# Kernel tuning notes

Measured on AMD Instinct MI355X. Metric: run time of the kernel, lower is better.

Reference implementation:

```python
import jax, jax.numpy as jnp
import numpy as np

N = 16384      # number of PF candidates (nodes)
D_IN = 13      # pfc_input_dim
H = 16         # hidden_dim
K = 8          # kNN neighbors (includes self, dist 0, matching PyG knn(x, x, k))


def setup_inputs() -> dict:
    key = jax.random.key(0)
    ks = jax.random.split(key, 8)

    def w(k, shape):
        return (jax.random.normal(k, shape, dtype=jnp.float32) * 0.1)

    z = lambda n: jnp.zeros((n,), dtype=jnp.float32)
    return {
        "x_pfc": jax.random.normal(ks[0], (N, D_IN), dtype=jnp.float32),
        # pfc_encode: Linear(13,8) SiLU, Linear(8,16) SiLU, Linear(16,15)
        "W1": w(ks[1], (D_IN, H // 2)), "b1": z(H // 2),
        "W2": w(ks[2], (H // 2, H)),    "b2": z(H),
        "W3": w(ks[3], (H, H - 1)),     "b3": z(H - 1),
        # DynamicEdgeConv edge MLP: Linear(2H, H) SiLU
        "We": w(ks[4], (2 * H, H)),     "be": z(H),
        # ffn: Linear(H, 2H) SiLU, Linear(2H, H)
        "Wf1": w(ks[5], (H, 2 * H)),    "bf1": z(2 * H),
        "Wf2": w(ks[6], (2 * H, H)),    "bf2": z(H),
    }


def reference(x_pfc, W1, b1, W2, b2, W3, b3, We, be, Wf1, bf1, Wf2, bf2):
    silu = jax.nn.silu
    # pfc_encode (dropout = identity in eval)
    h = silu(x_pfc @ W1 + b1)
    h = silu(h @ W2 + b2)
    h = h @ W3 + b3                                   # [N, H-1]
    x = jnp.concatenate([h, x_pfc[:, -1:]], axis=1)   # [N, H]

    # Dynamic kNN graph in encoded-feature space (self included, dist 0)
    sq = jnp.sum(x * x, axis=1)                       # [N]
    d2 = sq[:, None] + sq[None, :] - 2.0 * (x @ x.T)  # [N, N] pairwise sq dist
    _, idx = jax.lax.top_k(-d2, K)                    # [N, K] neighbor indices

    # EdgeConv message: nn(cat([x_i, x_j - x_i])), mean aggregation
    x_j = x[idx]                                      # [N, K, H] gather
    x_i = x[:, None, :]                               # [N, 1, H]
    edge_in = jnp.concatenate(
        [jnp.broadcast_to(x_i, x_j.shape), x_j - x_i], axis=-1)  # [N, K, 2H]
    msg = silu(edge_in @ We + be)                     # [N, K, H]
    feats = jnp.mean(msg, axis=1)                     # [N, H]

    # ffn (dropout = identity in eval)
    f = silu(feats @ Wf1 + bf1)
    f = f @ Wf2 + bf2                                 # [N, H]
    return jnp.concatenate([f, x_pfc], axis=1)        # [N, H + D_IN]
```

## Files before the change

kernel.cpp:

```cpp
#include <hip/hip_runtime.h>
#include <math.h>

#define NPTS 16384
#define DIN 13
#define KNN 8
#define GL 12
#define BIGF 1.7014118e38f

typedef _Float16 half8 __attribute__((ext_vector_type(8)));
typedef float f32x4 __attribute__((ext_vector_type(4)));
typedef float f32x16 __attribute__((ext_vector_type(16)));

union HU4 { uint4 u; half8 h; };

__device__ __forceinline__ float silu(float v) {
    return v / (1.0f + __expf(-v));
}

#define MED3(v, a, b) __builtin_amdgcn_fmed3f((v), (a), (b))

#define INS8V(v) {                      \
    d7 = MED3((v), d6, d7);             \
    d6 = MED3((v), d5, d6);             \
    d5 = MED3((v), d4, d5);             \
    d4 = MED3((v), d3, d4);             \
    d3 = MED3((v), d2, d3);             \
    d2 = MED3((v), d1, d2);             \
    d1 = MED3((v), d0, d1);             \
    d0 = fminf((v), d0); }

#define INS12G(v) {                     \
    g11 = MED3((v), g10, g11);          \
    g10 = MED3((v), g9, g10);           \
    g9  = MED3((v), g8, g9);            \
    g8  = MED3((v), g7, g8);            \
    g7  = MED3((v), g6, g7);            \
    g6  = MED3((v), g5, g6);            \
    g5  = MED3((v), g4, g5);            \
    g4  = MED3((v), g3, g4);            \
    g3  = MED3((v), g2, g3);            \
    g2  = MED3((v), g1, g2);            \
    g1  = MED3((v), g0, g1);            \
    g0  = fminf((v), g0); }

#define CSW(p, q) { float lo_ = fminf(m##p, m##q); float hi_ = fmaxf(m##p, m##q); m##p = lo_; m##q = hi_; }

#define CLEAN16() \
    CSW(0,8) CSW(1,9) CSW(2,10) CSW(3,11) CSW(4,12) CSW(5,13) CSW(6,14) CSW(7,15) \
    CSW(0,4) CSW(1,5) CSW(2,6) CSW(3,7) CSW(8,12) CSW(9,13) CSW(10,14) CSW(11,15) \
    CSW(0,2) CSW(1,3) CSW(4,6) CSW(5,7) CSW(8,10) CSW(9,11) CSW(12,14) CSW(13,15) \
    CSW(0,1) CSW(2,3) CSW(4,5) CSW(6,7) CSW(8,9) CSW(10,11) CSW(12,13) CSW(14,15)

#define MERGE12_SHFL(mask) {                                  \
    float b0 = __shfl_xor(g0, (mask), 64);                    \
    float b1 = __shfl_xor(g1, (mask), 64);                    \
    float b2 = __shfl_xor(g2, (mask), 64);                    \
    float b3 = __shfl_xor(g3, (mask), 64);                    \
    float b4 = __shfl_xor(g4, (mask), 64);                    \
    float b5 = __shfl_xor(g5, (mask), 64);                    \
    float b6 = __shfl_xor(g6, (mask), 64);                    \
    float b7 = __shfl_xor(g7, (mask), 64);                    \
    float b8 = __shfl_xor(g8, (mask), 64);                    \
    float b9 = __shfl_xor(g9, (mask), 64);                    \
    float b10 = __shfl_xor(g10, (mask), 64);                  \
    float b11 = __shfl_xor(g11, (mask), 64);                  \
    float m0 = g0, m1 = g1, m2 = g2, m3 = g3;                 \
    float m4 = fminf(g4, b11), m5 = fminf(g5, b10);           \
    float m6 = fminf(g6, b9),  m7 = fminf(g7, b8);            \
    float m8 = fminf(g8, b7),  m9 = fminf(g9, b6);            \
    float m10 = fminf(g10, b5), m11 = fminf(g11, b4);         \
    float m12 = b3, m13 = b2, m14 = b1, m15 = b0;             \
    CLEAN16();                                                \
    g0 = m0; g1 = m1; g2 = m2; g3 = m3; g4 = m4; g5 = m5;     \
    g6 = m6; g7 = m7; g8 = m8; g9 = m9; g10 = m10; g11 = m11; }

#define MERGE12_LDS(LD) {                                     \
    float b0 = LD(0), b1 = LD(1), b2 = LD(2), b3 = LD(3);     \
    float b4 = LD(4), b5 = LD(5), b6 = LD(6), b7 = LD(7);     \
    float b8 = LD(8), b9 = LD(9), b10 = LD(10), b11 = LD(11); \
    float m0 = g0, m1 = g1, m2 = g2, m3 = g3;                 \
    float m4 = fminf(g4, b11), m5 = fminf(g5, b10);           \
    float m6 = fminf(g6, b9),  m7 = fminf(g7, b8);            \
    float m8 = fminf(g8, b7),  m9 = fminf(g9, b6);            \
    float m10 = fminf(g10, b5), m11 = fminf(g11, b4);         \
    float m12 = b3, m13 = b2, m14 = b1, m15 = b0;             \
    CLEAN16();                                                \
    g0 = m0; g1 = m1; g2 = m2; g3 = m3; g4 = m4; g5 = m5;     \
    g6 = m6; g7 = m7; g8 = m8; g9 = m9; g10 = m10; g11 = m11; }

#define MERGE8(mask) {                                   \
    float b0 = __shfl_xor(d0, (mask), 64);               \
    float b1 = __shfl_xor(d1, (mask), 64);               \
    float b2 = __shfl_xor(d2, (mask), 64);               \
    float b3 = __shfl_xor(d3, (mask), 64);               \
    float b4 = __shfl_xor(d4, (mask), 64);               \
    float b5 = __shfl_xor(d5, (mask), 64);               \
    float b6 = __shfl_xor(d6, (mask), 64);               \
    float b7 = __shfl_xor(d7, (mask), 64);               \
    float m0 = fminf(d0, b7), m1 = fminf(d1, b6);        \
    float m2 = fminf(d2, b5), m3 = fminf(d3, b4);        \
    float m4 = fminf(d4, b3), m5 = fminf(d5, b2);        \
    float m6 = fminf(d6, b1), m7 = fminf(d7, b0);        \
    CSW(0,4) CSW(1,5) CSW(2,6) CSW(3,7)                  \
    CSW(0,2) CSW(1,3) CSW(4,6) CSW(5,7)                  \
    CSW(0,1) CSW(2,3) CSW(4,5) CSW(6,7)                  \
    d0 = m0; d1 = m1; d2 = m2; d3 = m3;                  \
    d4 = m4; d5 = m5; d6 = m6; d7 = m7; }

__global__ __launch_bounds__(64) void k_encoder(
    const float* __restrict__ x_pfc,
    const float* __restrict__ W1, const float* __restrict__ b1,
    const float* __restrict__ W2, const float* __restrict__ b2,
    const float* __restrict__ W3, const float* __restrict__ b3,
    const float* __restrict__ We, const float* __restrict__ be,
    float* __restrict__ xo, _Float16* __restrict__ H, _Float16* __restrict__ L,
    _Float16* __restrict__ YH, _Float16* __restrict__ YL,
    float* __restrict__ SQF, unsigned* __restrict__ SQHL,
    float* __restrict__ ACC)
{
    __shared__ float sW1[DIN * 8];
    __shared__ float sb1[8];
    __shared__ float sW2[8 * 16];
    __shared__ float sb2[16];
    __shared__ float sW3[16 * 15];
    __shared__ float sb3[15];
    __shared__ float sWe[16 * 16];
    __shared__ float sbe[16];
    int t = threadIdx.x;
    for (int q = t; q < DIN * 8; q += 64) sW1[q] = W1[q];
    for (int q = t; q < 8; q += 64) sb1[q] = b1[q];
    for (int q = t; q < 8 * 16; q += 64) sW2[q] = W2[q];
    for (int q = t; q < 16; q += 64) sb2[q] = b2[q];
    for (int q = t; q < 16 * 15; q += 64) sW3[q] = W3[q];
    for (int q = t; q < 15; q += 64) sb3[q] = b3[q];
    for (int q = t; q < 16 * 16; q += 64) sWe[q] = We[q];
    for (int q = t; q < 16; q += 64) sbe[q] = be[q];
    __syncthreads();

    int i = blockIdx.x * 64 + t;
    float in[DIN];
#pragma unroll
    for (int d = 0; d < DIN; ++d) in[d] = x_pfc[i * DIN + d];

    float a1[8];
#pragma unroll
    for (int h = 0; h < 8; ++h) a1[h] = sb1[h];
#pragma unroll
    for (int d = 0; d < DIN; ++d) {
        float v = in[d];
#pragma unroll
        for (int h = 0; h < 8; ++h) a1[h] += v * sW1[d * 8 + h];
    }
#pragma unroll
    for (int h = 0; h < 8; ++h) a1[h] = silu(a1[h]);

    float a2[16];
#pragma unroll
    for (int h = 0; h < 16; ++h) a2[h] = sb2[h];
#pragma unroll
    for (int d = 0; d < 8; ++d) {
        float v = a1[d];
#pragma unroll
        for (int h = 0; h < 16; ++h) a2[h] += v * sW2[d * 16 + h];
    }
#pragma unroll
    for (int h = 0; h < 16; ++h) a2[h] = silu(a2[h]);

    float a3[15];
#pragma unroll
    for (int h = 0; h < 15; ++h) a3[h] = sb3[h];
#pragma unroll
    for (int d = 0; d < 16; ++d) {
        float v = a2[d];
#pragma unroll
        for (int h = 0; h < 15; ++h) a3[h] += v * sW3[d * 15 + h];
    }

    float xr[16];
#pragma unroll
    for (int h = 0; h < 15; ++h) xr[h] = a3[h];
    xr[15] = in[DIN - 1];

    float s = 0.0f;
#pragma unroll
    for (int d = 0; d < 16; ++d) s += xr[d] * xr[d];

    float accb[16];
#pragma unroll
    for (int h = 0; h < 16; ++h) accb[h] = sbe[h];
#pragma unroll
    for (int d = 0; d < 16; ++d) {
        float v = xr[d];
#pragma unroll
        for (int h = 0; h < 16; ++h) accb[h] += v * sWe[d * 16 + h];
    }

    _Float16 hb[16], lb[16], yhb[16], ylb[16];
#pragma unroll
    for (int d = 0; d < 16; ++d) {
        _Float16 h = (_Float16)xr[d];
        hb[d] = h;
        lb[d] = (_Float16)(xr[d] - (float)h);
        float y = -2.0f * xr[d];
        _Float16 yh = (_Float16)y;
        yhb[d] = yh;
        ylb[d] = (_Float16)(y - (float)yh);
    }
    {
        uint4* p;
        p = (uint4*)(H + (size_t)i * 16);  p[0] = ((uint4*)hb)[0];  p[1] = ((uint4*)hb)[1];
        p = (uint4*)(L + (size_t)i * 16);  p[0] = ((uint4*)lb)[0];  p[1] = ((uint4*)lb)[1];
        p = (uint4*)(YH + (size_t)i * 16); p[0] = ((uint4*)yhb)[0]; p[1] = ((uint4*)yhb)[1];
        p = (uint4*)(YL + (size_t)i * 16); p[0] = ((uint4*)ylb)[0]; p[1] = ((uint4*)ylb)[1];
        f32x4* xq = (f32x4*)(xo + (size_t)i * 16);
        f32x4* aq = (f32x4*)(ACC + (size_t)i * 16);
#pragma unroll
        for (int q = 0; q < 4; ++q) {
            f32x4 xv, av;
#pragma unroll
            for (int r = 0; r < 4; ++r) { xv[r] = xr[q * 4 + r]; av[r] = accb[q * 4 + r]; }
            xq[q] = xv;
            aq[q] = av;
        }
    }
    SQF[i] = s;
    {
        _Float16 sh = (_Float16)s;
        _Float16 sl = (_Float16)(s - (float)sh);
        unsigned uh = *(const unsigned short*)&sh;
        unsigned ul = *(const unsigned short*)&sl;
        SQHL[i] = (ul << 16) | uh;
    }
}

__global__ __launch_bounds__(512, 4) void k_knn(
    const _Float16* __restrict__ H, const _Float16* __restrict__ L,
    const _Float16* __restrict__ YH, const _Float16* __restrict__ YL,
    const unsigned* __restrict__ SQHL, unsigned* __restrict__ CV)
{
    __shared__ float wl[8 * GL * 32];

    int t = threadIdx.x;
    int w = t >> 6;
    int lane = t & 63;
    int r31 = lane & 31;
    int hh = lane >> 5;
    int ih = blockIdx.x >> 1;
    int jh = blockIdx.x & 1;
    int i0 = ih * 32;

    int gi = i0 + r31;
    half8 B1 = *(const half8*)(YH + (size_t)gi * 16 + hh * 8);
    half8 B2 = *(const half8*)(YL + (size_t)gi * 16 + hh * 8);
    half8 B4;
    {
        HU4 r;
        r.u.x = (hh == 0) ? 0x3C003C00u : 0u;
        r.u.y = 0u; r.u.z = 0u; r.u.w = 0u;
        B4 = r.h;
    }
    unsigned sqmask = (hh == 0) ? 0xFFFFFFFFu : 0u;

    float g0 = BIGF, g1 = BIGF, g2 = BIGF, g3 = BIGF;
    float g4 = BIGF, g5 = BIGF, g6 = BIGF, g7 = BIGF;
    float g8 = BIGF, g9 = BIGF, g10 = BIGF, g11 = BIGF;

    int jw = jh * 8192 + w * 1024;
    const _Float16* pH = H + ((size_t)(jw + r31)) * 16 + hh * 8;
    const _Float16* pL = L + ((size_t)(jw + r31)) * 16 + hh * 8;
    const unsigned* pQ = SQHL + jw + r31;
    unsigned idt0 = (unsigned)((w << 1) | hh);

#pragma unroll 4
    for (int tt = 0; tt < 32; ++tt) {
        half8 Ah = *(const half8*)(pH + (size_t)tt * 512);
        half8 Al = *(const half8*)(pL + (size_t)tt * 512);
        unsigned squ = pQ[tt * 32];
        HU4 a4;
        a4.u.x = squ & sqmask;
        a4.u.y = 0u; a4.u.z = 0u; a4.u.w = 0u;

        f32x16 c = {};
        c = __builtin_amdgcn_mfma_f32_32x32x16_f16(a4.h, B4, c, 0, 0, 0);
        c = __builtin_amdgcn_mfma_f32_32x32x16_f16(Ah, B1, c, 0, 0, 0);
        c = __builtin_amdgcn_mfma_f32_32x32x16_f16(Al, B1, c, 0, 0, 0);
        c = __builtin_amdgcn_mfma_f32_32x32x16_f16(Ah, B2, c, 0, 0, 0);

        float v0 = fminf(fminf(c[0], c[1]), c[2]);
        float v1 = fminf(fminf(c[3], c[4]), c[5]);
        float v2 = fminf(fminf(c[6], c[7]), c[8]);
        float v3 = fminf(fminf(c[9], c[10]), c[11]);
        float v4 = fminf(fminf(c[12], c[13]), c[14]);
        float v5 = fminf(fminf(v0, v1), c[15]);
        float v6 = fminf(fminf(v2, v3), v4);
        float vmin = fminf(v5, v6);

        unsigned pk = (__float_as_uint(vmin) & 0xFFFFFC00u) | (idt0 + (unsigned)(tt << 4));
        float pf = __uint_as_float(pk);
        INS12G(pf);
    }

    MERGE12_SHFL(32);

#define STORE12() if (lane < 32) {                     \
        wl[(w * GL + 0) * 32 + r31] = g0;              \
        wl[(w * GL + 1) * 32 + r31] = g1;              \
        wl[(w * GL + 2) * 32 + r31] = g2;              \
        wl[(w * GL + 3) * 32 + r31] = g3;              \
        wl[(w * GL + 4) * 32 + r31] = g4;              \
        wl[(w * GL + 5) * 32 + r31] = g5;              \
        wl[(w * GL + 6) * 32 + r31] = g6;              \
        wl[(w * GL + 7) * 32 + r31] = g7;              \
        wl[(w * GL + 8) * 32 + r31] = g8;              \
        wl[(w * GL + 9) * 32 + r31] = g9;              \
        wl[(w * GL + 10) * 32 + r31] = g10;            \
        wl[(w * GL + 11) * 32 + r31] = g11; }

    if (w >= 4) STORE12();
    __syncthreads();
    if (w < 4) {
        int pw = w + 4;
#define LD(s) wl[(pw * GL + (s)) * 32 + r31]
        MERGE12_LDS(LD);
#undef LD
    }
    __syncthreads();
    if (w == 2 || w == 3) STORE12();
    __syncthreads();
    if (w < 2) {
        int pw = w + 2;
#define LD(s) wl[(pw * GL + (s)) * 32 + r31]
        MERGE12_LDS(LD);
#undef LD
    }
    __syncthreads();
    if (w == 1) STORE12();
    __syncthreads();
    if (w == 0) {
        int pw = 1;
#define LD(s) wl[(pw * GL + (s)) * 32 + r31]
        MERGE12_LDS(LD);
#undef LD
        if (lane < 32) {
            unsigned jb = ((unsigned)jh) << 9;
            size_t base = ((size_t)jh * NPTS + (i0 + r31)) * GL;
            CV[base + 0] = __float_as_uint(g0) | jb;
            CV[base + 1] = __float_as_uint(g1) | jb;
            CV[base + 2] = __float_as_uint(g2) | jb;
            CV[base + 3] = __float_as_uint(g3) | jb;
            CV[base + 4] = __float_as_uint(g4) | jb;
            CV[base + 5] = __float_as_uint(g5) | jb;
            CV[base + 6] = __float_as_uint(g6) | jb;
            CV[base + 7] = __float_as_uint(g7) | jb;
            CV[base + 8] = __float_as_uint(g8) | jb;
            CV[base + 9] = __float_as_uint(g9) | jb;
            CV[base + 10] = __float_as_uint(g10) | jb;
            CV[base + 11] = __float_as_uint(g11) | jb;
        }
    }
#undef STORE12
}

__global__ __launch_bounds__(512, 4) void k_head(
    const float* __restrict__ x, const unsigned* __restrict__ CV,
    const float* __restrict__ SQF,
    const float* __restrict__ x_pfc, const float* __restrict__ ACC,
    const float* __restrict__ We,
    const float* __restrict__ Wf1, const float* __restrict__ bf1,
    const float* __restrict__ Wf2, const float* __restrict__ bf2,
    float* __restrict__ out)
{
    __shared__ float sWe2[16 * 16];
    __shared__ float sWf1[16 * 32];
    __shared__ float sbf1[32];
    __shared__ float sWf2[32 * 16];
    __shared__ float sbf2[16];
    __shared__ int sGrp[32][GL];
    __shared__ int cnt[32];
    __shared__ int sIdx[32 * 8];
    __shared__ float sF1[32 * 33];
    int t = threadIdx.x;
    for (int q = t; q < 16 * 16; q += 512) sWe2[q] = We[256 + q];
    for (int q = t; q < 16 * 32; q += 512) sWf1[q] = Wf1[q];
    for (int q = t; q < 32; q += 512) sbf1[q] = bf1[q];
    for (int q = t; q < 32 * 16; q += 512) sWf2[q] = Wf2[q];
    for (int q = t; q < 16; q += 512) sbf2[q] = bf2[q];

    int i0 = blockIdx.x * 32;

    if (t < 64) {
        int pi = t & 31;
        int hf = t >> 5;
        const f32x4* c = (const f32x4*)(CV + ((size_t)hf * NPTS + (i0 + pi)) * GL);
        f32x4 c0 = c[0], c1 = c[1], c2 = c[2];
        float g0 = c0[0], g1 = c0[1], g2 = c0[2], g3 = c0[3];
        float g4 = c1[0], g5 = c1[1], g6 = c1[2], g7 = c1[3];
        float g8 = c2[0], g9 = c2[1], g10 = c2[2], g11 = c2[3];
        MERGE12_SHFL(32);
        if (t < 32) {
            cnt[pi] = 0;
#define DECJB(gk, s) { unsigned id_ = __float_as_uint(gk) & 0x3FFu;          \
            sGrp[pi][s] = (int)(((id_ >> 9) & 1) * 8192 + ((id_ >> 1) & 7) * 1024 + \
                                ((id_ >> 4) & 31) * 32 + (id_ & 1) * 4); }
            DECJB(g0, 0) DECJB(g1, 1) DECJB(g2, 2) DECJB(g3, 3)
            DECJB(g4, 4) DECJB(g5, 5) DECJB(g6, 6) DECJB(g7, 7)
            DECJB(g8, 8) DECJB(g9, 9) DECJB(g10, 10) DECJB(g11, 11)
#undef DECJB
        }
    }
    __syncthreads();

    int l = t & 15;
    int pt = t >> 4;
    int ql = l & 3;
    int qd = l >> 2;
    int i = i0 + pt;

    float xi[16];
    {
        const f32x4* xiv = (const f32x4*)(x + (size_t)i * 16);
#pragma unroll
        for (int q = 0; q < 4; ++q) {
            f32x4 a = xiv[q];
#pragma unroll
            for (int r = 0; r < 4; ++r) xi[q * 4 + r] = a[r];
        }
    }
    f32x4 xiq = ((const f32x4*)(x + (size_t)i * 16))[ql];

    float val[12];
    float d0 = BIGF, d1 = BIGF, d2 = BIGF, d3 = BIGF;
    float d4 = BIGF, d5 = BIGF, d6 = BIGF, d7 = BIGF;
#pragma unroll
    for (int g = 0; g < GL; ++g) {
        int jb = sGrp[pt][g];
        float vg = BIGF;
#pragma unroll
        for (int rho = 0; rho < 4; ++rho) {
            f32x4 a = *((const f32x4*)(x + ((size_t)(jb + rho * 8)) * 16) + l);
            float qdot = xiq[0] * a[0];
            qdot = fmaf(xiq[1], a[1], qdot);
            qdot = fmaf(xiq[2], a[2], qdot);
            qdot = fmaf(xiq[3], a[3], qdot);
            qdot += __shfl_xor(qdot, 1, 64);
            qdot += __shfl_xor(qdot, 2, 64);
            float v = fmaf(qdot, -2.0f, SQF[jb + rho * 8 + qd]);
            vg = (ql == rho) ? v : vg;
        }
        val[g] = vg;
        INS8V(vg);
    }

    MERGE8(1);
    MERGE8(2);
    MERGE8(4);
    MERGE8(8);
    float kth = d7;

#pragma unroll
    for (int g = 0; g < GL; ++g) {
        float v = val[g];
        if (v <= kth) {
            int j = sGrp[pt][g] + ql * 8 + qd;
            int p = atomicAdd(&cnt[pt], 1);
            if (p < KNN) sIdx[pt * 8 + p] = j;
        }
    }
    __syncthreads();

    int e8 = l & 7;
    int j = sIdx[pt * 8 + e8];

    float xd[16];
    {
        const f32x4* xjv = (const f32x4*)(x + (size_t)j * 16);
#pragma unroll
        for (int q = 0; q < 4; ++q) {
            f32x4 a = xjv[q];
#pragma unroll
            for (int r = 0; r < 4; ++r) xd[q * 4 + r] = a[r] - xi[q * 4 + r];
        }
    }

    float acc[16];
    {
        const f32x4* av = (const f32x4*)(ACC + (size_t)i * 16);
#pragma unroll
        for (int q = 0; q < 4; ++q) {
            f32x4 a = av[q];
#pragma unroll
            for (int r = 0; r < 4; ++r) acc[q * 4 + r] = a[r];
        }
    }
#pragma unroll
    for (int d = 0; d < 16; ++d) {
        float v = xd[d];
#pragma unroll
        for (int h = 0; h < 16; ++h) acc[h] += v * sWe2[d * 16 + h];
    }

    float feats[16];
#pragma unroll
    for (int h = 0; h < 16; ++h) feats[h] = silu(acc[h]);

#pragma unroll
    for (int mask = 1; mask <= 4; mask <<= 1) {
#pragma unroll
        for (int h = 0; h < 16; ++h) feats[h] += __shfl_xor(feats[h], mask, 64);
    }
#pragma unroll
    for (int h = 0; h < 16; ++h) feats[h] *= 0.125f;

    float p0 = sbf1[l];
    float p1 = sbf1[l + 16];
#pragma unroll
    for (int k = 0; k < 16; ++k) {
        float v = feats[k];
        p0 = fmaf(v, sWf1[k * 32 + l], p0);
        p1 = fmaf(v, sWf1[k * 32 + l + 16], p1);
    }
    p0 = silu(p0);
    p1 = silu(p1);
    sF1[pt * 33 + l] = p0;
    sF1[pt * 33 + 16 + l] = p1;
    __syncthreads();

    float o = sbf2[l];
#pragma unroll
    for (int k = 0; k < 32; ++k)
        o = fmaf(sF1[pt * 33 + k], sWf2[k * 16 + l], o);

    out[(size_t)i * 29 + l] = o;
    if (l < DIN) out[(size_t)i * 29 + 16 + l] = x_pfc[i * DIN + l];
}

extern "C" void kernel_launch(void* const* d_in, const int* in_sizes, int n_in,
                              void* d_out, int out_size, void* d_ws, size_t ws_size,
                              hipStream_t stream)
{
    const float* x_pfc = (const float*)d_in[0];
    const float* W1 = (const float*)d_in[1];
    const float* b1 = (const float*)d_in[2];
    const float* W2 = (const float*)d_in[3];
    const float* b2 = (const float*)d_in[4];
    const float* W3 = (const float*)d_in[5];
    const float* b3 = (const float*)d_in[6];
    const float* We = (const float*)d_in[7];
    const float* be = (const float*)d_in[8];
    const float* Wf1 = (const float*)d_in[9];
    const float* bf1 = (const float*)d_in[10];
    const float* Wf2 = (const float*)d_in[11];
    const float* bf2 = (const float*)d_in[12];
    float* out = (float*)d_out;

    float* xw = (float*)d_ws;
    float* ACCa = xw + (size_t)NPTS * 16;
    _Float16* Ha = (_Float16*)(ACCa + (size_t)NPTS * 16);
    _Float16* La = Ha + (size_t)NPTS * 16;
    _Float16* YHa = La + (size_t)NPTS * 16;
    _Float16* YLa = YHa + (size_t)NPTS * 16;
    float* SQFa = (float*)(YLa + (size_t)NPTS * 16);
    unsigned* SQHLa = (unsigned*)(SQFa + NPTS);
    unsigned* CVa = SQHLa + NPTS;

    hipLaunchKernelGGL(k_encoder, dim3(NPTS / 64), dim3(64), 0, stream,
                       x_pfc, W1, b1, W2, b2, W3, b3, We, be,
                       xw, Ha, La, YHa, YLa, SQFa, SQHLa, ACCa);
    hipLaunchKernelGGL(k_knn, dim3(NPTS / 32 * 2), dim3(512), 0, stream,
                       Ha, La, YHa, YLa, SQHLa, CVa);
    hipLaunchKernelGGL(k_head, dim3(NPTS / 32), dim3(512), 0, stream,
                       xw, CVa, SQFa, x_pfc, ACCa, We, Wf1, bf1, Wf2, bf2, out);
}
```

Before: 152.7 us.

## Seed kNN MFMA accumulator with squared norms from LDS instead of extra MFMA

```diff
diff --git a/kernel.cpp b/kernel.cpp
--- a/kernel.cpp
+++ b/kernel.cpp
@@ -236,9 +236,9 @@
 __global__ __launch_bounds__(512, 4) void k_knn(
     const _Float16* __restrict__ H, const _Float16* __restrict__ L,
     const _Float16* __restrict__ YH, const _Float16* __restrict__ YL,
-    const unsigned* __restrict__ SQHL, unsigned* __restrict__ CV)
+    const float* __restrict__ SQF, unsigned* __restrict__ CV)
 {
-    __shared__ float wl[8 * GL * 32];
+    __shared__ float sBuf[8192];
 
     int t = threadIdx.x;
     int w = t >> 6;
@@ -252,14 +252,12 @@
     int gi = i0 + r31;
     half8 B1 = *(const half8*)(YH + (size_t)gi * 16 + hh * 8);
     half8 B2 = *(const half8*)(YL + (size_t)gi * 16 + hh * 8);
-    half8 B4;
+
     {
-        HU4 r;
-        r.u.x = (hh == 0) ? 0x3C003C00u : 0u;
-        r.u.y = 0u; r.u.z = 0u; r.u.w = 0u;
-        B4 = r.h;
-    }
-    unsigned sqmask = (hh == 0) ? 0xFFFFFFFFu : 0u;
+        const f32x4* src = (const f32x4*)(SQF + jh * 8192);
+        f32x4* dst = (f32x4*)sBuf;
+        for (int q = t; q < 2048; q += 512) dst[q] = src[q];
+    }
 
     float g0 = BIGF, g1 = BIGF, g2 = BIGF, g3 = BIGF;
     float g4 = BIGF, g5 = BIGF, g6 = BIGF, g7 = BIGF;
@@ -268,59 +266,80 @@
     int jw = jh * 8192 + w * 1024;
     const _Float16* pH = H + ((size_t)(jw + r31)) * 16 + hh * 8;
     const _Float16* pL = L + ((size_t)(jw + r31)) * 16 + hh * 8;
-    const unsigned* pQ = SQHL + jw + r31;
-    unsigned idt0 = (unsigned)((w << 1) | hh);
-
-#pragma unroll 4
-    for (int tt = 0; tt < 32; ++tt) {
-        half8 Ah = *(const half8*)(pH + (size_t)tt * 512);
-        half8 Al = *(const half8*)(pL + (size_t)tt * 512);
-        unsigned squ = pQ[tt * 32];
-        HU4 a4;
-        a4.u.x = squ & sqmask;
-        a4.u.y = 0u; a4.u.z = 0u; a4.u.w = 0u;
-
-        f32x16 c = {};
-        c = __builtin_amdgcn_mfma_f32_32x32x16_f16(a4.h, B4, c, 0, 0, 0);
-        c = __builtin_amdgcn_mfma_f32_32x32x16_f16(Ah, B1, c, 0, 0, 0);
-        c = __builtin_amdgcn_mfma_f32_32x32x16_f16(Al, B1, c, 0, 0, 0);
-        c = __builtin_amdgcn_mfma_f32_32x32x16_f16(Ah, B2, c, 0, 0, 0);
-
-        float v0 = fminf(fminf(c[0], c[1]), c[2]);
-        float v1 = fminf(fminf(c[3], c[4]), c[5]);
-        float v2 = fminf(fminf(c[6], c[7]), c[8]);
-        float v3 = fminf(fminf(c[9], c[10]), c[11]);
-        float v4 = fminf(fminf(c[12], c[13]), c[14]);
-        float v5 = fminf(fminf(v0, v1), c[15]);
-        float v6 = fminf(fminf(v2, v3), v4);
-        float vmin = fminf(v5, v6);
-
-        unsigned pk = (__float_as_uint(vmin) & 0xFFFFFC00u) | (idt0 + (unsigned)(tt << 4));
-        float pf = __uint_as_float(pk);
-        INS12G(pf);
+    const float* sqb = sBuf + w * 1024 + hh * 4;
+    unsigned idt = (unsigned)((w << 1) | hh);
+
+    __syncthreads();
+
+#pragma unroll 1
+    for (int cc = 0; cc < 8; ++cc) {
+        half8 Ah0 = *(const half8*)(pH);
+        half8 Al0 = *(const half8*)(pL);
+        half8 Ah1 = *(const half8*)(pH + 512);
+        half8 Al1 = *(const half8*)(pL + 512);
+        half8 Ah2 = *(const half8*)(pH + 1024);
+        half8 Al2 = *(const half8*)(pL + 1024);
+        half8 Ah3 = *(const half8*)(pH + 1536);
+        half8 Al3 = *(const half8*)(pL + 1536);
+        const float* sq4 = sqb + cc * 128;
+        unsigned idc = idt + (unsigned)(cc << 6);
+
+#define TILE(AH, AL, U) {                                                    \
+        const f32x4* s_ = (const f32x4*)(sq4 + (U) * 32);                    \
+        f32x4 s0 = s_[0], s1 = s_[2], s2 = s_[4], s3 = s_[6];                \
+        f32x16 c;                                                            \
+        c[0] = s0[0]; c[1] = s0[1]; c[2] = s0[2]; c[3] = s0[3];              \
+        c[4] = s1[0]; c[5] = s1[1]; c[6] = s1[2]; c[7] = s1[3];              \
+        c[8] = s2[0]; c[9] = s2[1]; c[10] = s2[2]; c[11] = s2[3];            \
+        c[12] = s3[0]; c[13] = s3[1]; c[14] = s3[2]; c[15] = s3[3];          \
+        c = __builtin_amdgcn_mfma_f32_32x32x16_f16(AH, B1, c, 0, 0, 0);      \
+        c = __builtin_amdgcn_mfma_f32_32x32x16_f16(AL, B1, c, 0, 0, 0);      \
+        c = __builtin_amdgcn_mfma_f32_32x32x16_f16(AH, B2, c, 0, 0, 0);      \
+        float v0 = fminf(fminf(c[0], c[1]), c[2]);                           \
+        float v1 = fminf(fminf(c[3], c[4]), c[5]);                           \
+        float v2 = fminf(fminf(c[6], c[7]), c[8]);                           \
+        float v3 = fminf(fminf(c[9], c[10]), c[11]);                         \
+        float v4 = fminf(fminf(c[12], c[13]), c[14]);                        \
+        float v5 = fminf(fminf(v0, v1), c[15]);                              \
+        float v6 = fminf(fminf(v2, v3), v4);                                 \
+        float vmin = fminf(v5, v6);                                          \
+        unsigned pk = (__float_as_uint(vmin) & 0xFFFFFC00u)                  \
+                    | (idc + (unsigned)((U) << 4));                          \
+        float pf = __uint_as_float(pk);                                      \
+        INS12G(pf); }
+
+        TILE(Ah0, Al0, 0)
+        TILE(Ah1, Al1, 1)
+        TILE(Ah2, Al2, 2)
+        TILE(Ah3, Al3, 3)
+#undef TILE
+        pH += 2048;
+        pL += 2048;
     }
 
     MERGE12_SHFL(32);
 
-#define STORE12() if (lane < 32) {                     \
-        wl[(w * GL + 0) * 32 + r31] = g0;              \
-        wl[(w * GL + 1) * 32 + r31] = g1;              \
-        wl[(w * GL + 2) * 32 + r31] = g2;              \
-        wl[(w * GL + 3) * 32 + r31] = g3;              \
-        wl[(w * GL + 4) * 32 + r31] = g4;              \
-        wl[(w * GL + 5) * 32 + r31] = g5;              \
-        wl[(w * GL + 6) * 32 + r31] = g6;              \
-        wl[(w * GL + 7) * 32 + r31] = g7;              \
-        wl[(w * GL + 8) * 32 + r31] = g8;              \
-        wl[(w * GL + 9) * 32 + r31] = g9;              \
-        wl[(w * GL + 10) * 32 + r31] = g10;            \
-        wl[(w * GL + 11) * 32 + r31] = g11; }
+    __syncthreads();
+
+#define STORE12() if (lane < 32) {                       \
+        sBuf[(w * GL + 0) * 32 + r31] = g0;              \
+        sBuf[(w * GL + 1) * 32 + r31] = g1;              \
+        sBuf[(w * GL + 2) * 32 + r31] = g2;              \
+        sBuf[(w * GL + 3) * 32 + r31] = g3;              \
+        sBuf[(w * GL + 4) * 32 + r31] = g4;              \
+        sBuf[(w * GL + 5) * 32 + r31] = g5;              \
+        sBuf[(w * GL + 6) * 32 + r31] = g6;              \
+        sBuf[(w * GL + 7) * 32 + r31] = g7;              \
+        sBuf[(w * GL + 8) * 32 + r31] = g8;              \
+        sBuf[(w * GL + 9) * 32 + r31] = g9;              \
+        sBuf[(w * GL + 10) * 32 + r31] = g10;            \
+        sBuf[(w * GL + 11) * 32 + r31] = g11; }
 
     if (w >= 4) STORE12();
     __syncthreads();
     if (w < 4) {
         int pw = w + 4;
-#define LD(s) wl[(pw * GL + (s)) * 32 + r31]
+#define LD(s) sBuf[(pw * GL + (s)) * 32 + r31]
         MERGE12_LDS(LD);
 #undef LD
     }
@@ -329,7 +348,7 @@
     __syncthreads();
     if (w < 2) {
         int pw = w + 2;
-#define LD(s) wl[(pw * GL + (s)) * 32 + r31]
+#define LD(s) sBuf[(pw * GL + (s)) * 32 + r31]
         MERGE12_LDS(LD);
 #undef LD
     }
@@ -338,7 +357,7 @@
     __syncthreads();
     if (w == 0) {
         int pw = 1;
-#define LD(s) wl[(pw * GL + (s)) * 32 + r31]
+#define LD(s) sBuf[(pw * GL + (s)) * 32 + r31]
         MERGE12_LDS(LD);
 #undef LD
         if (lane < 32) {
@@ -567,7 +586,7 @@
                        x_pfc, W1, b1, W2, b2, W3, b3, We, be,
                        xw, Ha, La, YHa, YLa, SQFa, SQHLa, ACCa);
     hipLaunchKernelGGL(k_knn, dim3(NPTS / 32 * 2), dim3(512), 0, stream,
-                       Ha, La, YHa, YLa, SQHLa, CVa);
+                       Ha, La, YHa, YLa, SQFa, CVa);
     hipLaunchKernelGGL(k_head, dim3(NPTS / 32), dim3(512), 0, stream,
                        xw, CVa, SQFa, x_pfc, ACCa, We, Wf1, bf1, Wf2, bf2, out);
 }
```

After: 152.9 us. No clear change (+0.1%).

## Process two query tiles per kNN block and preload squared norms into LDS

Applied to the files above, without the earlier changes.

```diff
diff --git a/kernel.cpp b/kernel.cpp
--- a/kernel.cpp
+++ b/kernel.cpp
@@ -12,6 +12,7 @@
 typedef float f32x16 __attribute__((ext_vector_type(16)));
 
 union HU4 { uint4 u; half8 h; };
+union C16 { f32x16 w; f32x4 q[4]; };
 
 __device__ __forceinline__ float silu(float v) {
     return v / (1.0f + __expf(-v));
@@ -29,19 +30,21 @@
     d1 = MED3((v), d0, d1);             \
     d0 = fminf((v), d0); }
 
-#define INS12G(v) {                     \
-    g11 = MED3((v), g10, g11);          \
-    g10 = MED3((v), g9, g10);           \
-    g9  = MED3((v), g8, g9);            \
-    g8  = MED3((v), g7, g8);            \
-    g7  = MED3((v), g6, g7);            \
-    g6  = MED3((v), g5, g6);            \
-    g5  = MED3((v), g4, g5);            \
-    g4  = MED3((v), g3, g4);            \
-    g3  = MED3((v), g2, g3);            \
-    g2  = MED3((v), g1, g2);            \
-    g1  = MED3((v), g0, g1);            \
-    g0  = fminf((v), g0); }
+#define INS12L(G, v) {                  \
+    G##11 = MED3((v), G##10, G##11);    \
+    G##10 = MED3((v), G##9, G##10);     \
+    G##9  = MED3((v), G##8, G##9);      \
+    G##8  = MED3((v), G##7, G##8);      \
+    G##7  = MED3((v), G##6, G##7);      \
+    G##6  = MED3((v), G##5, G##6);      \
+    G##5  = MED3((v), G##4, G##5);      \
+    G##4  = MED3((v), G##3, G##4);      \
+    G##3  = MED3((v), G##2, G##3);      \
+    G##2  = MED3((v), G##1, G##2);      \
+    G##1  = MED3((v), G##0, G##1);      \
+    G##0  = fminf((v), G##0); }
+
+#define INS12G(v) INS12L(g, v)
 
 #define CSW(p, q) { float lo_ = fminf(m##p, m##q); float hi_ = fmaxf(m##p, m##q); m##p = lo_; m##q = hi_; }
 
@@ -51,42 +54,48 @@
     CSW(0,2) CSW(1,3) CSW(4,6) CSW(5,7) CSW(8,10) CSW(9,11) CSW(12,14) CSW(13,15) \
     CSW(0,1) CSW(2,3) CSW(4,5) CSW(6,7) CSW(8,9) CSW(10,11) CSW(12,13) CSW(14,15)
 
-#define MERGE12_SHFL(mask) {                                  \
-    float b0 = __shfl_xor(g0, (mask), 64);                    \
-    float b1 = __shfl_xor(g1, (mask), 64);                    \
-    float b2 = __shfl_xor(g2, (mask), 64);                    \
-    float b3 = __shfl_xor(g3, (mask), 64);                    \
-    float b4 = __shfl_xor(g4, (mask), 64);                    \
-    float b5 = __shfl_xor(g5, (mask), 64);                    \
-    float b6 = __shfl_xor(g6, (mask), 64);                    \
-    float b7 = __shfl_xor(g7, (mask), 64);                    \
-    float b8 = __shfl_xor(g8, (mask), 64);                    \
-    float b9 = __shfl_xor(g9, (mask), 64);                    \
-    float b10 = __shfl_xor(g10, (mask), 64);                  \
-    float b11 = __shfl_xor(g11, (mask), 64);                  \
-    float m0 = g0, m1 = g1, m2 = g2, m3 = g3;                 \
-    float m4 = fminf(g4, b11), m5 = fminf(g5, b10);           \
-    float m6 = fminf(g6, b9),  m7 = fminf(g7, b8);            \
-    float m8 = fminf(g8, b7),  m9 = fminf(g9, b6);            \
-    float m10 = fminf(g10, b5), m11 = fminf(g11, b4);         \
+#define MERGE12_SHFLG(G, mask) {                              \
+    float b0 = __shfl_xor(G##0, (mask), 64);                  \
+    float b1 = __shfl_xor(G##1, (mask), 64);                  \
+    float b2 = __shfl_xor(G##2, (mask), 64);                  \
+    float b3 = __shfl_xor(G##3, (mask), 64);                  \
+    float b4 = __shfl_xor(G##4, (mask), 64);                  \
+    float b5 = __shfl_xor(G##5, (mask), 64);                  \
+    float b6 = __shfl_xor(G##6, (mask), 64);                  \
+    float b7 = __shfl_xor(G##7, (mask), 64);                  \
+    float b8 = __shfl_xor(G##8, (mask), 64);                  \
+    float b9 = __shfl_xor(G##9, (mask), 64);                  \
+    float b10 = __shfl_xor(G##10, (mask), 64);                \
+    float b11 = __shfl_xor(G##11, (mask), 64);                \
+    float m0 = G##0, m1 = G##1, m2 = G##2, m3 = G##3;         \
+    float m4 = fminf(G##4, b11), m5 = fminf(G##5, b10);       \
+    float m6 = fminf(G##6, b9),  m7 = fminf(G##7, b8);        \
+    float m8 = fminf(G##8, b7),  m9 = fminf(G##9, b6);        \
+    float m10 = fminf(G##10, b5), m11 = fminf(G##11, b4);     \
     float m12 = b3, m13 = b2, m14 = b1, m15 = b0;             \
     CLEAN16();                                                \
-    g0 = m0; g1 = m1; g2 = m2; g3 = m3; g4 = m4; g5 = m5;     \
-    g6 = m6; g7 = m7; g8 = m8; g9 = m9; g10 = m10; g11 = m11; }
-
-#define MERGE12_LDS(LD) {                                     \
+    G##0 = m0; G##1 = m1; G##2 = m2; G##3 = m3;               \
+    G##4 = m4; G##5 = m5; G##6 = m6; G##7 = m7;               \
+    G##8 = m8; G##9 = m9; G##10 = m10; G##11 = m11; }
+
+#define MERGE12_SHFL(mask) MERGE12_SHFLG(g, mask)
+
+#define MERGE12_LDSG(G, LD) {                                 \
     float b0 = LD(0), b1 = LD(1), b2 = LD(2), b3 = LD(3);     \
     float b4 = LD(4), b5 = LD(5), b6 = LD(6), b7 = LD(7);     \
     float b8 = LD(8), b9 = LD(9), b10 = LD(10), b11 = LD(11); \
-    float m0 = g0, m1 = g1, m2 = g2, m3 = g3;                 \
-    float m4 = fminf(g4, b11), m5 = fminf(g5, b10);           \
-    float m6 = fminf(g6, b9),  m7 = fminf(g7, b8);            \
-    float m8 = fminf(g8, b7),  m9 = fminf(g9, b6);            \
-    float m10 = fminf(g10, b5), m11 = fminf(g11, b4);         \
+    float m0 = G##0, m1 = G##1, m2 = G##2, m3 = G##3;         \
+    float m4 = fminf(G##4, b11), m5 = fminf(G##5, b10);       \
+    float m6 = fminf(G##6, b9),  m7 = fminf(G##7, b8);        \
+    float m8 = fminf(G##8, b7),  m9 = fminf(G##9, b6);        \
+    float m10 = fminf(G##10, b5), m11 = fminf(G##11, b4);     \
     float m12 = b3, m13 = b2, m14 = b1, m15 = b0;             \
     CLEAN16();                                                \
-    g0 = m0; g1 = m1; g2 = m2; g3 = m3; g4 = m4; g5 = m5;     \
-    g6 = m6; g7 = m7; g8 = m8; g9 = m9; g10 = m10; g11 = m11; }
+    G##0 = m0; G##1 = m1; G##2 = m2; G##3 = m3;               \
+    G##4 = m4; G##5 = m5; G##6 = m6; G##7 = m7;               \
+    G##8 = m8; G##9 = m9; G##10 = m10; G##11 = m11; }
+
+#define MERGE12_LDS(LD) MERGE12_LDSG(g, LD)
 
 #define MERGE8(mask) {                                   \
     float b0 = __shfl_xor(d0, (mask), 64);               \
@@ -236,9 +245,9 @@
 __global__ __launch_bounds__(512, 4) void k_knn(
     const _Float16* __restrict__ H, const _Float16* __restrict__ L,
     const _Float16* __restrict__ YH, const _Float16* __restrict__ YL,
-    const unsigned* __restrict__ SQHL, unsigned* __restrict__ CV)
+    const float* __restrict__ SQF, unsigned* __restrict__ CV)
 {
-    __shared__ float wl[8 * GL * 32];
+    __shared__ float sBuf[8192];
 
     int t = threadIdx.x;
     int w = t >> 6;
@@ -247,118 +256,188 @@
     int hh = lane >> 5;
     int ih = blockIdx.x >> 1;
     int jh = blockIdx.x & 1;
-    int i0 = ih * 32;
-
-    int gi = i0 + r31;
-    half8 B1 = *(const half8*)(YH + (size_t)gi * 16 + hh * 8);
-    half8 B2 = *(const half8*)(YL + (size_t)gi * 16 + hh * 8);
-    half8 B4;
+    int i0 = ih * 64;
+
+    int giA = i0 + r31;
+    int giB = i0 + 32 + r31;
+    half8 B1A = *(const half8*)(YH + (size_t)giA * 16 + hh * 8);
+    half8 B2A = *(const half8*)(YL + (size_t)giA * 16 + hh * 8);
+    half8 B1B = *(const half8*)(YH + (size_t)giB * 16 + hh * 8);
+    half8 B2B = *(const half8*)(YL + (size_t)giB * 16 + hh * 8);
+
     {
-        HU4 r;
-        r.u.x = (hh == 0) ? 0x3C003C00u : 0u;
-        r.u.y = 0u; r.u.z = 0u; r.u.w = 0u;
-        B4 = r.h;
-    }
-    unsigned sqmask = (hh == 0) ? 0xFFFFFFFFu : 0u;
-
-    float g0 = BIGF, g1 = BIGF, g2 = BIGF, g3 = BIGF;
-    float g4 = BIGF, g5 = BIGF, g6 = BIGF, g7 = BIGF;
-    float g8 = BIGF, g9 = BIGF, g10 = BIGF, g11 = BIGF;
+        const f32x4* src = (const f32x4*)(SQF + jh * 8192);
+        f32x4* dst = (f32x4*)sBuf;
+        for (int q = t; q < 2048; q += 512) dst[q] = src[q];
+    }
+
+    float gA0 = BIGF, gA1 = BIGF, gA2 = BIGF, gA3 = BIGF;
+    float gA4 = BIGF, gA5 = BIGF, gA6 = BIGF, gA7 = BIGF;
+    float gA8 = BIGF, gA9 = BIGF, gA10 = BIGF, gA11 = BIGF;
+    float gB0 = BIGF, gB1 = BIGF, gB2 = BIGF, gB3 = BIGF;
+    float gB4 = BIGF, gB5 = BIGF, gB6 = BIGF, gB7 = BIGF;
+    float gB8 = BIGF, gB9 = BIGF, gB10 = BIGF, gB11 = BIGF;
 
     int jw = jh * 8192 + w * 1024;
     const _Float16* pH = H + ((size_t)(jw + r31)) * 16 + hh * 8;
     const _Float16* pL = L + ((size_t)(jw + r31)) * 16 + hh * 8;
-    const unsigned* pQ = SQHL + jw + r31;
-    unsigned idt0 = (unsigned)((w << 1) | hh);
-
-#pragma unroll 4
+    const float* sqb = sBuf + w * 1024 + hh * 4;
+    unsigned idt = (unsigned)((w << 1) | hh);
+
+    __syncthreads();
+
+#pragma unroll 2
     for (int tt = 0; tt < 32; ++tt) {
         half8 Ah = *(const half8*)(pH + (size_t)tt * 512);
         half8 Al = *(const half8*)(pL + (size_t)tt * 512);
-        unsigned squ = pQ[tt * 32];
-        HU4 a4;
-        a4.u.x = squ & sqmask;
-        a4.u.y = 0u; a4.u.z = 0u; a4.u.w = 0u;
-
-        f32x16 c = {};
-        c = __builtin_amdgcn_mfma_f32_32x32x16_f16(a4.h, B4, c, 0, 0, 0);
-        c = __builtin_amdgcn_mfma_f32_32x32x16_f16(Ah, B1, c, 0, 0, 0);
-        c = __builtin_amdgcn_mfma_f32_32x32x16_f16(Al, B1, c, 0, 0, 0);
-        c = __builtin_amdgcn_mfma_f32_32x32x16_f16(Ah, B2, c, 0, 0, 0);
-
-        float v0 = fminf(fminf(c[0], c[1]), c[2]);
-        float v1 = fminf(fminf(c[3], c[4]), c[5]);
-        float v2 = fminf(fminf(c[6], c[7]), c[8]);
-        float v3 = fminf(fminf(c[9], c[10]), c[11]);
-        float v4 = fminf(fminf(c[12], c[13]), c[14]);
-        float v5 = fminf(fminf(v0, v1), c[15]);
-        float v6 = fminf(fminf(v2, v3), v4);
-        float vmin = fminf(v5, v6);
-
-        unsigned pk = (__float_as_uint(vmin) & 0xFFFFFC00u) | (idt0 + (unsigned)(tt << 4));
-        float pf = __uint_as_float(pk);
-        INS12G(pf);
-    }
-
-    MERGE12_SHFL(32);
-
-#define STORE12() if (lane < 32) {                     \
-        wl[(w * GL + 0) * 32 + r31] = g0;              \
-        wl[(w * GL + 1) * 32 + r31] = g1;              \
-        wl[(w * GL + 2) * 32 + r31] = g2;              \
-        wl[(w * GL + 3) * 32 + r31] = g3;              \
-        wl[(w * GL + 4) * 32 + r31] = g4;              \
-        wl[(w * GL + 5) * 32 + r31] = g5;              \
-        wl[(w * GL + 6) * 32 + r31] = g6;              \
-        wl[(w * GL + 7) * 32 + r31] = g7;              \
-        wl[(w * GL + 8) * 32 + r31] = g8;              \
-        wl[(w * GL + 9) * 32 + r31] = g9;              \
-        wl[(w * GL + 10) * 32 + r31] = g10;            \
-        wl[(w * GL + 11) * 32 + r31] = g11; }
-
-    if (w >= 4) STORE12();
+        const f32x4* s_ = (const f32x4*)(sqb + tt * 32);
+        f32x4 s0 = s_[0], s1 = s_[2], s2 = s_[4], s3 = s_[6];
+
+        C16 cA, cB;
+        cA.q[0] = s0; cA.q[1] = s1; cA.q[2] = s2; cA.q[3] = s3;
+        cB.q[0] = s0; cB.q[1] = s1; cB.q[2] = s2; cB.q[3] = s3;
+        cA.w = __builtin_amdgcn_mfma_f32_32x32x16_f16(Ah, B1A, cA.w, 0, 0, 0);
+        cB.w = __builtin_amdgcn_mfma_f32_32x32x16_f16(Ah, B1B, cB.w, 0, 0, 0);
+        cA.w = __builtin_amdgcn_mfma_f32_32x32x16_f16(Al, B1A, cA.w, 0, 0, 0);
+        cB.w = __builtin_amdgcn_mfma_f32_32x32x16_f16(Al, B1B, cB.w, 0, 0, 0);
+        cA.w = __builtin_amdgcn_mfma_f32_32x32x16_f16(Ah, B2A, cA.w, 0, 0, 0);
+        cB.w = __builtin_amdgcn_mfma_f32_32x32x16_f16(Ah, B2B, cB.w, 0, 0, 0);
+
+        unsigned idc = idt + (unsigned)(tt << 4);
+        {
+            float v0 = fminf(fminf(cA.w[0], cA.w[1]), cA.w[2]);
+            float v1 = fminf(fminf(cA.w[3], cA.w[4]), cA.w[5]);
+            float v2 = fminf(fminf(cA.w[6], cA.w[7]), cA.w[8]);
+            float v3 = fminf(fminf(cA.w[9], cA.w[10]), cA.w[11]);
+            float v4 = fminf(fminf(cA.w[12], cA.w[13]), cA.w[14]);
+            float v5 = fminf(fminf(v0, v1), cA.w[15]);
+            float v6 = fminf(fminf(v2, v3), v4);
+            float vmin = fminf(v5, v6);
+            unsigned pk = (__float_as_uint(vmin) & 0xFFFFFC00u) | idc;
+            float pf = __uint_as_float(pk);
+            INS12L(gA, pf);
+        }
+        {
+            float v0 = fminf(fminf(cB.w[0], cB.w[1]), cB.w[2]);
+            float v1 = fminf(fminf(cB.w[3], cB.w[4]), cB.w[5]);
+            float v2 = fminf(fminf(cB.w[6], cB.w[7]), cB.w[8]);
+            float v3 = fminf(fminf(cB.w[9], cB.w[10]), cB.w[11]);
+            float v4 = fminf(fminf(cB.w[12], cB.w[13]), cB.w[14]);
+            float v5 = fminf(fminf(v0, v1), cB.w[15]);
+            float v6 = fminf(fminf(v2, v3), v4);
+            float vmin = fminf(v5, v6);
+            unsigned pk = (__float_as_uint(vmin) & 0xFFFFFC00u) | idc;
+            float pf = __uint_as_float(pk);
+            INS12L(gB, pf);
+        }
+    }
+
+    MERGE12_SHFLG(gA, 32);
+    MERGE12_SHFLG(gB, 32);
+
+    __syncthreads();
+
+#define STORE24() if (lane < 32) {                         \
+        sBuf[(w * 24 + 0) * 32 + r31] = gA0;               \
+        sBuf[(w * 24 + 1) * 32 + r31] = gA1;               \
+        sBuf[(w * 24 + 2) * 32 + r31] = gA2;               \
+        sBuf[(w * 24 + 3) * 32 + r31] = gA3;               \
+        sBuf[(w * 24 + 4) * 32 + r31] = gA4;               \
+        sBuf[(w * 24 + 5) * 32 + r31] = gA5;               \
+        sBuf[(w * 24 + 6) * 32 + r31] = gA6;               \
+        sBuf[(w * 24 + 7) * 32 + r31] = gA7;               \
+        sBuf[(w * 24 + 8) * 32 + r31] = gA8;               \
+        sBuf[(w * 24 + 9) * 32 + r31] = gA9;               \
+        sBuf[(w * 24 + 10) * 32 + r31] = gA10;             \
+        sBuf[(w * 24 + 11) * 32 + r31] = gA11;             \
+        sBuf[(w * 24 + 12) * 32 + r31] = gB0;              \
+        sBuf[(w * 24 + 13) * 32 + r31] = gB1;              \
+        sBuf[(w * 24 + 14) * 32 + r31] = gB2;              \
+        sBuf[(w * 24 + 15) * 32 + r31] = gB3;              \
+        sBuf[(w * 24 + 16) * 32 + r31] = gB4;              \
+        sBuf[(w * 24 + 17) * 32 + r31] = gB5;              \
+        sBuf[(w * 24 + 18) * 32 + r31] = gB6;              \
+        sBuf[(w * 24 + 19) * 32 + r31] = gB7;              \
+        sBuf[(w * 24 + 20) * 32 + r31] = gB8;              \
+        sBuf[(w * 24 + 21) * 32 + r31] = gB9;              \
+        sBuf[(w * 24 + 22) * 32 + r31] = gB10;             \
+        sBuf[(w * 24 + 23) * 32 + r31] = gB11; }
+
+#define MERGE_STEP(pw) {                                   \
+        int pw_ = (pw);                                    \
+        const float* mb = sBuf + (pw_ * 24) * 32 + r31;    \
+        { _Pragma("clang diagnostic push")                 \
+          ; }                                              \
+        {                                                  \
+        }                                                  \
+    }
+
+    if (w >= 4) STORE24();
     __syncthreads();
     if (w < 4) {
         int pw = w + 4;
-#define LD(s) wl[(pw * GL + (s)) * 32 + r31]
-        MERGE12_LDS(LD);
-#undef LD
-    }
-    __syncthreads();
-    if (w == 2 || w == 3) STORE12();
+#define LDA(s) sBuf[(pw * 24 + (s)) * 32 + r31]
+#define LDB(s) sBuf[(pw * 24 + 12 + (s)) * 32 + r31]
+        MERGE12_LDSG(gA, LDA);
+        MERGE12_LDSG(gB, LDB);
+#undef LDA
+#undef LDB
+    }
+    __syncthreads();
+    if (w == 2 || w == 3) STORE24();
     __syncthreads();
     if (w < 2) {
         int pw = w + 2;
-#define LD(s) wl[(pw * GL + (s)) * 32 + r31]
-        MERGE12_LDS(LD);
-#undef LD
-    }
-    __syncthreads();
-    if (w == 1) STORE12();
+#define LDA(s) sBuf[(pw * 24 + (s)) * 32 + r31]
+#define LDB(s) sBuf[(pw * 24 + 12 + (s)) * 32 + r31]
+        MERGE12_LDSG(gA, LDA);
+        MERGE12_LDSG(gB, LDB);
+#undef LDA
+#undef LDB
+    }
+    __syncthreads();
+    if (w == 1) STORE24();
     __syncthreads();
     if (w == 0) {
         int pw = 1;
-#define LD(s) wl[(pw * GL + (s)) * 32 + r31]
-        MERGE12_LDS(LD);
-#undef LD
+#define LDA(s) sBuf[(pw * 24 + (s)) * 32 + r31]
+#define LDB(s) sBuf[(pw * 24 + 12 + (s)) * 32 + r31]
+        MERGE12_LDSG(gA, LDA);
+        MERGE12_LDSG(gB, LDB);
+#undef LDA
+#undef LDB
         if (lane < 32) {
             unsigned jb = ((unsigned)jh) << 9;
-            size_t base = ((size_t)jh * NPTS + (i0 + r31)) * GL;
-            CV[base + 0] = __float_as_uint(g0) | jb;
-            CV[base + 1] = __float_as_uint(g1) | jb;
-            CV[base + 2] = __float_as_uint(g2) | jb;
-            CV[base + 3] = __float_as_uint(g3) | jb;
-            CV[base + 4] = __float_as_uint(g4) | jb;
-            CV[base + 5] = __float_as_uint(g5) | jb;
-            CV[base + 6] = __float_as_uint(g6) | jb;
-            CV[base + 7] = __float_as_uint(g7) | jb;
-            CV[base + 8] = __float_as_uint(g8) | jb;
-            CV[base + 9] = __float_as_uint(g9) | jb;
-            CV[base + 10] = __float_as_uint(g10) | jb;
-            CV[base + 11] = __float_as_uint(g11) | jb;
-        }
-    }
-#undef STORE12
+            size_t baseA = ((size_t)jh * NPTS + (i0 + r31)) * GL;
+            size_t baseB = ((size_t)jh * NPTS + (i0 + 32 + r31)) * GL;
+            CV[baseA + 0] = __float_as_uint(gA0) | jb;
+            CV[baseA + 1] = __float_as_uint(gA1) | jb;
+            CV[baseA + 2] = __float_as_uint(gA2) | jb;
+            CV[baseA + 3] = __float_as_uint(gA3) | jb;
+            CV[baseA + 4] = __float_as_uint(gA4) | jb;
+            CV[baseA + 5] = __float_as_uint(gA5) | jb;
+            CV[baseA + 6] = __float_as_uint(gA6) | jb;
+            CV[baseA + 7] = __float_as_uint(gA7) | jb;
+            CV[baseA + 8] = __float_as_uint(gA8) | jb;
+            CV[baseA + 9] = __float_as_uint(gA9) | jb;
+            CV[baseA + 10] = __float_as_uint(gA10) | jb;
+            CV[baseA + 11] = __float_as_uint(gA11) | jb;
+            CV[baseB + 0] = __float_as_uint(gB0) | jb;
+            CV[baseB + 1] = __float_as_uint(gB1) | jb;
+            CV[baseB + 2] = __float_as_uint(gB2) | jb;
+            CV[baseB + 3] = __float_as_uint(gB3) | jb;
+            CV[baseB + 4] = __float_as_uint(gB4) | jb;
+            CV[baseB + 5] = __float_as_uint(gB5) | jb;
+            CV[baseB + 6] = __float_as_uint(gB6) | jb;
+            CV[baseB + 7] = __float_as_uint(gB7) | jb;
+            CV[baseB + 8] = __float_as_uint(gB8) | jb;
+            CV[baseB + 9] = __float_as_uint(gB9) | jb;
+            CV[baseB + 10] = __float_as_uint(gB10) | jb;
+            CV[baseB + 11] = __float_as_uint(gB11) | jb;
+        }
+    }
+#undef STORE24
+#undef MERGE_STEP
 }
 
 __global__ __launch_bounds__(512, 4) void k_head(
@@ -566,8 +645,8 @@
     hipLaunchKernelGGL(k_encoder, dim3(NPTS / 64), dim3(64), 0, stream,
                        x_pfc, W1, b1, W2, b2, W3, b3, We, be,
                        xw, Ha, La, YHa, YLa, SQFa, SQHLa, ACCa);
-    hipLaunchKernelGGL(k_knn, dim3(NPTS / 32 * 2), dim3(512), 0, stream,
-                       Ha, La, YHa, YLa, SQHLa, CVa);
+    hipLaunchKernelGGL(k_knn, dim3(NPTS / 64 * 2), dim3(512), 0, stream,
+                       Ha, La, YHa, YLa, SQFa, CVa);
     hipLaunchKernelGGL(k_head, dim3(NPTS / 32), dim3(512), 0, stream,
                        xw, CVa, SQFa, x_pfc, ACCa, We, Wf1, bf1, Wf2, bf2, out);
 }
```

After: 150.3 us. Within noise of the previous version (-1.6%).
